# Kernel tuning notes

Hardware: AMD Instinct MI355X
Metric: run time of the kernel (lower is better)

Reference implementation:

```python
import jax, jax.numpy as jnp
import numpy as np

B, S, D, H, KV, HD = 2, 2048, 1024, 16, 4, 64
NUM_BUCKETS, MAX_DIST = 32, 128


def _rel_pos_bucket(rel_pos, num_buckets=NUM_BUCKETS, max_distance=MAX_DIST):
    # bidirectional (is_decoder=False) T5 bucketing
    nb = num_buckets // 2
    buckets = (rel_pos > 0).astype(jnp.int32) * nb
    rel = jnp.abs(rel_pos)
    max_exact = nb // 2
    is_small = rel < max_exact
    rel_f = jnp.maximum(rel, 1).astype(jnp.float32)
    large = max_exact + (
        jnp.log(rel_f / max_exact) / np.log(max_distance / max_exact) * (nb - max_exact)
    ).astype(jnp.int32)
    large = jnp.minimum(large, nb - 1)
    return buckets + jnp.where(is_small, rel, large)


def _pool_weight(W, scale, apply_scale):
    # W: [inner_dim, d_model] (torch Linear layout). Optionally scale per head,
    # group-sum heads into kv_heads, broadcast back to n_heads.
    Wh = W.reshape(H, HD, D)                       # [H, hd, D]
    if apply_scale:
        # torch path: W.T -> [D,H,hd] * scale[H,1] -> back; equivalent per-head scale
        Wh = Wh * scale[:, :, None]                # scale: [H,1] -> [H,1,1]
    Wg = Wh.reshape(KV, H // KV, HD, D).sum(axis=1)  # [KV, hd, D]
    Wb = jnp.repeat(Wg, H // KV, axis=0)           # [H, hd, D]
    return Wb.reshape(H * HD, D)


def setup_inputs() -> dict:
    key = jax.random.key(0)
    ks = jax.random.split(key, 8)
    s = 1.0 / np.sqrt(D)
    return {
        "hidden_states": jax.random.normal(ks[0], (B, S, D), jnp.float32),
        "Wq": jax.random.normal(ks[1], (H * HD, D), jnp.float32) * s,
        "Wk": jax.random.normal(ks[2], (H * HD, D), jnp.float32) * s,
        "Wv": jax.random.normal(ks[3], (H * HD, D), jnp.float32) * s,
        "Wo": jax.random.normal(ks[4], (D, H * HD), jnp.float32) * s,
        "key_scale": jax.random.normal(ks[5], (H, 1), jnp.float32),
        "value_scale": jax.random.normal(ks[6], (H, 1), jnp.float32),
        "bias_emb": jax.random.normal(ks[7], (NUM_BUCKETS, H), jnp.float32),
    }


def reference(hidden_states, Wq, Wk, Wv, Wo, key_scale, value_scale, bias_emb):
    x = hidden_states
    # Q projection -> [B, H, S, hd]
    q = (x @ Wq.T).reshape(B, S, H, HD).transpose(0, 2, 1, 3)

    # K weight: per-head scale applied, then pooled. V weight: the original code
    # computes the scaled version but then (bug, replicated faithfully) pools the
    # RAW v weight, so value_scale has no effect on the forward math.
    Wk_eff = _pool_weight(Wk, key_scale, apply_scale=True)
    Wv_eff = _pool_weight(Wv, value_scale, apply_scale=False)

    k = (x @ Wk_eff.T).reshape(B, S, H, HD).transpose(0, 2, 1, 3)
    v = (x @ Wv_eff.T).reshape(B, S, H, HD).transpose(0, 2, 1, 3)

    # T5 attention: no 1/sqrt(d) scaling
    scores = jnp.einsum("bhqd,bhkd->bhqk", q, k)  # [B,H,S,S]

    # relative position bias
    ctx = jnp.arange(S)[:, None]
    mem = jnp.arange(S)[None, :]
    buckets = _rel_pos_bucket(mem - ctx)            # [S, S]
    pos_bias = bias_emb[buckets]                    # [S, S, H]
    pos_bias = pos_bias.transpose(2, 0, 1)[None]    # [1, H, S, S]

    scores = scores + pos_bias
    attn = jax.nn.softmax(scores.astype(jnp.float32), axis=-1).astype(scores.dtype)
    out = jnp.einsum("bhqk,bhkd->bhqd", attn, v)    # [B,H,S,hd]
    out = out.transpose(0, 2, 1, 3).reshape(B, S, H * HD)
    return out @ Wo.T                               # [B, S, D]
```

## Files before the change

### kernel.cpp

```cpp
#include <hip/hip_runtime.h>

using half8  = __attribute__((ext_vector_type(8))) _Float16;
using half4  = __attribute__((ext_vector_type(4))) _Float16;
using half2v = __attribute__((ext_vector_type(2))) _Float16;
using fp16x2 = __attribute__((ext_vector_type(2))) __fp16;
using f32x4  = __attribute__((ext_vector_type(4))) float;

#define BB 2
#define SS 2048
#define DD 1024
#define HH 16
#define KVH 4
#define HDIM 64
#define NQK 1280
#define LOG2E 1.4426950408889634f

#define GLDS(g, l) __builtin_amdgcn_global_load_lds( \
    (const __attribute__((address_space(1))) void*)(g), \
    (__attribute__((address_space(3))) void*)(l), 16, 0, 0)

__device__ __forceinline__ f32x4 mfma16(half4 a, half4 b, f32x4 c) {
    return __builtin_amdgcn_mfma_f32_16x16x16f16(a, b, c, 0, 0, 0);
}

__device__ __forceinline__ float fexp2(float x) {
#if __has_builtin(__builtin_amdgcn_exp2f)
    return __builtin_amdgcn_exp2f(x);
#else
    return exp2f(x);
#endif
}

__device__ __forceinline__ half2v cvt_pk_f16(float a, float b) {
    fp16x2 r = __builtin_amdgcn_cvt_pkrtz(a, b);
    return __builtin_bit_cast(half2v, r);
}

__device__ __forceinline__ int kv_off(int row, int hcol) {
    return row * 64 + ((((hcol >> 3) ^ row) & 7) << 3) + (hcol & 7);
}

__device__ __forceinline__ int gm_off(int row, int slot) {
    return row * 32 + (((slot ^ row) & 3) << 3);
}

__device__ __forceinline__ int rel_large(int rel) {
    int n;
    if (rel < 12) n = 0; else if (rel < 16) n = 1; else if (rel < 23) n = 2;
    else if (rel < 32) n = 3; else if (rel < 46) n = 4; else if (rel < 64) n = 5;
    else if (rel < 91) n = 6; else if (rel < 128) n = 7; else n = 8;
    int large = 8 + n;
    return large > 15 ? 15 : large;
}

__global__ void prep_all(const float* __restrict__ x,
                         const float* __restrict__ Wq, const float* __restrict__ Wk,
                         const float* __restrict__ Wv, const float* __restrict__ Wo,
                         const float* __restrict__ ksc, const float* __restrict__ bias_emb,
                         _Float16* __restrict__ Wqk, _Float16* __restrict__ Wvb,
                         _Float16* __restrict__ Wob, float* __restrict__ tab,
                         _Float16* __restrict__ Xh)
{
    int bid = blockIdx.x;
    if (bid < 2560) {
        int row = bid;
        int c = threadIdx.x * 4;
        if (row < NQK) {
            if (row < 1024) {
                #pragma unroll
                for (int j = 0; j < 4; ++j)
                    Wqk[(size_t)row * DD + c + j] = (_Float16)(Wq[(size_t)row * DD + c + j] * LOG2E);
            } else {
                int kh = row - 1024;
                int kvi = kh >> 6, hd = kh & 63;
                #pragma unroll
                for (int j = 0; j < 4; ++j) {
                    float s = 0.f;
                    #pragma unroll
                    for (int g = 0; g < 4; ++g)
                        s += Wk[(size_t)((kvi * 4 + g) * 64 + hd) * DD + c + j] * ksc[kvi * 4 + g];
                    Wqk[(size_t)row * DD + c + j] = (_Float16)s;
                }
            }
        } else if (row < 1536) {
            int vh = row - 1280;
            int kvi = vh >> 6, hd = vh & 63;
            #pragma unroll
            for (int j = 0; j < 4; ++j) {
                float s = 0.f;
                #pragma unroll
                for (int g = 0; g < 4; ++g)
                    s += Wv[(size_t)((kvi * 4 + g) * 64 + hd) * DD + c + j];
                Wvb[(size_t)vh * DD + c + j] = (_Float16)s;
            }
        } else {
            int r = row - 1536;
            #pragma unroll
            for (int j = 0; j < 4; ++j)
                Wob[(size_t)r * DD + c + j] = (_Float16)Wo[(size_t)r * DD + c + j];
        }
    } else if (bid < 6656) {
        int idx = ((bid - 2560) * 256 + threadIdx.x) * 4;
        float4 v = *(const float4*)(x + idx);
        half4 o = { (_Float16)v.x, (_Float16)v.y, (_Float16)v.z, (_Float16)v.w };
        *(half4*)(Xh + idx) = o;
    } else {
        int idx = (bid - 6656) * 256 + threadIdx.x;
        if (idx < HH * 4095) {
            int h = idx / 4095;
            int dpos = idx % 4095;
            int d = dpos - 2047;
            int rel = d < 0 ? -d : d;
            int bucket = (rel < 8) ? rel : rel_large(rel);
            if (d > 0) bucket += 16;
            tab[(size_t)h * 4095 + dpos] = bias_emb[bucket * HH + h] * LOG2E;
        }
    }
}

template<int OUTK>
__global__ __launch_bounds__(256) void gemm_bt(const _Float16* __restrict__ A,
                                               const _Float16* __restrict__ B,
                                               void* __restrict__ C0,
                                               _Float16* __restrict__ C1,
                                               int M, int K, int ldc)
{
    __shared__ __align__(16) _Float16 As[2][64 * 32];
    __shared__ __align__(16) _Float16 Bs[2][128 * 32];

    int nwg = gridDim.x * gridDim.y;
    int lid = blockIdx.y * gridDim.x + blockIdx.x;
    int sid = (lid & 7) * (nwg >> 3) + (lid >> 3);
    int m0 = (sid / gridDim.x) * 64, n0 = (sid % gridDim.x) * 128;

    int t = threadIdx.x;
    int wv = t >> 6, lane = t & 63;
    int wm = wv >> 1, wn = wv & 1;
    int lr = lane & 15, lg = lane >> 4;
    int srow = lane >> 2;
    int scol = (((lane & 3) ^ (srow & 3)) << 3);
    f32x4 acc[2][4] = {};

#define GSTAGE(BUF, K0)                                                       \
    {                                                                         \
                         \
        GLDS(A + (size_t)(m0 + wv * 16 + srow) * K + (K0) + scol,             \
             &As[BUF][wv * 512 + lane * 8]);                                  \
        _Pragma("unroll")                                                     \
        for (int i_ = 0; i_ < 2; ++i_) {                                      \
            int chunk_ = wv * 2 + i_;                                         \
            GLDS(B + (size_t)(n0 + chunk_ * 16 + srow) * K + (K0) + scol,     \
                 &Bs[BUF][chunk_ * 512 + lane * 8]);                          \
        }                                                                     \
    }

    GSTAGE(0, 0);
    __syncthreads();
    int cur = 0;

    for (int k0 = 0; k0 < K; k0 += 32) {
        if (k0 + 32 < K) GSTAGE(cur ^ 1, k0 + 32);
        half8 af[2], bfr[4];
        #pragma unroll
        for (int mi = 0; mi < 2; ++mi)
            af[mi] = *(const half8*)(&As[cur][gm_off(wm * 32 + mi * 16 + lr, lg)]);
        #pragma unroll
        for (int ni = 0; ni < 4; ++ni)
            bfr[ni] = *(const half8*)(&Bs[cur][gm_off(wn * 64 + ni * 16 + lr, lg)]);
        __builtin_amdgcn_s_setprio(1);
        #pragma unroll
        for (int mi = 0; mi < 2; ++mi)
            #pragma unroll
            for (int ni = 0; ni < 4; ++ni)
                acc[mi][ni] = __builtin_amdgcn_mfma_f32_16x16x32_f16(af[mi], bfr[ni], acc[mi][ni], 0, 0, 0);
        __builtin_amdgcn_s_setprio(0);
        __syncthreads();
        cur ^= 1;
    }
#undef GSTAGE

    #pragma unroll
    for (int mi = 0; mi < 2; ++mi) {
        #pragma unroll
        for (int ni = 0; ni < 4; ++ni) {
            int rowb = m0 + wm * 32 + mi * 16 + 4 * lg;
            int col  = n0 + wn * 64 + ni * 16 + lr;
            if constexpr (OUTK == 0) {
                #pragma unroll
                for (int r = 0; r < 4; ++r)
                    ((float*)C0)[(size_t)(rowb + r) * ldc + col] = acc[mi][ni][r];
            } else {
                if (n0 < 1280) {
                    #pragma unroll
                    for (int r = 0; r < 4; ++r)
                        ((_Float16*)C0)[(size_t)(rowb + r) * ldc + col] = (_Float16)acc[mi][ni][r];
                } else {
                    half4 o = { (_Float16)acc[mi][ni][0], (_Float16)acc[mi][ni][1],
                                (_Float16)acc[mi][ni][2], (_Float16)acc[mi][ni][3] };
                    *(half4*)(C1 + (size_t)(col - 1280) * M + rowb) = o;
                }
            }
        }
    }
}

__global__ __launch_bounds__(512) void attn(const _Float16* __restrict__ Y,
                                            const _Float16* __restrict__ Vt,
                                            const float* __restrict__ tab,
                                            _Float16* __restrict__ O)
{
    int blk = (blockIdx.x & 7) * 64 + (blockIdx.x >> 3);
    int qb = blk & 15, h = (blk >> 4) & 15, b = blk >> 8;
    int kv = h >> 2;
    int q0 = qb * 128;
    int t = threadIdx.x, w = t >> 6, lane = t & 63, lr = lane & 15, lg = lane >> 4;

    __shared__ __align__(16) _Float16 Ks[2][64 * 64];
    __shared__ __align__(16) _Float16 Vst[2][64 * 64];
    __shared__ float bias_s[2][192];

    const size_t yoff = (size_t)(b * SS + q0 + w * 16 + lr) * NQK + h * 64;
    half8 aq0 = *(const half8*)(Y + yoff + lg * 8);
    half8 aq1 = *(const half8*)(Y + yoff + 32 + lg * 8);

    const float bias_neg = tab[(size_t)h * 4095 + 0];
    const float bias_pos = tab[(size_t)h * 4095 + 4094];

    f32x4 acc_o[4] = {};
    float m = -1e30f, l = 0.f;
    const int bb = 127 - w * 16 - lr + 4 * lg;

    uint4 kreg, vreg;
    float breg = 0.f;
    const int srow = t >> 3, sc8 = (t & 7) << 3;

#define FAR(K0) (((K0) >= q0 + 256) || ((K0) <= q0 - 192))

#define ATTN_LOAD(KEY0)                                                          \
    {                                                                            \
        int k0_ = (KEY0);                                                        \
        kreg = *(const uint4*)(Y + (size_t)(b * SS + k0_ + srow) * NQK + 1024 + kv * 64 + sc8); \
        vreg = *(const uint4*)(Vt + (size_t)(kv * 64 + srow) * 4096 + b * SS + k0_ + sc8); \
        if (!FAR(k0_) && t < 192) {                                              \
            int ti = k0_ - q0 + t + 1920;                                        \
            ti = ti < 0 ? 0 : (ti > 4094 ? 4094 : ti);                           \
            breg = tab[(size_t)h * 4095 + ti];                                   \
        }                                                                        \
    }

#define ATTN_WRITE(BUF, KEY0)                                                    \
    {                                                                            \
        int bf_ = (BUF);                                                         \
        *(uint4*)(&Ks[bf_][kv_off(srow, sc8)]) = kreg;                           \
        *(uint4*)(&Vst[bf_][kv_off(srow, sc8)]) = vreg;                          \
        if (!FAR(KEY0) && t < 192) bias_s[bf_][t] = breg;                        \
    }

    ATTN_LOAD(0);
    ATTN_WRITE(0, 0);
    __syncthreads();
    int cur = 0;

    for (int key0 = 0; key0 < SS; key0 += 64) {
        if (key0 + 64 < SS) ATTN_LOAD(key0 + 64);

        const _Float16* ks = Ks[cur];
        const _Float16* vs = Vst[cur];
        bool far = FAR(key0);

        f32x4 z = {0.f, 0.f, 0.f, 0.f};
        f32x4 sc[4];
        __builtin_amdgcn_s_setprio(1);
        #pragma unroll
        for (int dt = 0; dt < 4; ++dt) {
            half8 bk0 = *(const half8*)(&ks[kv_off(dt * 16 + lr, lg * 8)]);
            half8 bk1 = *(const half8*)(&ks[kv_off(dt * 16 + lr, 32 + lg * 8)]);
            sc[dt] = __builtin_amdgcn_mfma_f32_16x16x32_f16(bk0, aq0, z, 0, 0, 0);
            sc[dt] = __builtin_amdgcn_mfma_f32_16x16x32_f16(bk1, aq1, sc[dt], 0, 0, 0);
        }
        __builtin_amdgcn_s_setprio(0);

        float c;
        if (!far) {
            #pragma unroll
            for (int dt = 0; dt < 4; ++dt)
                #pragma unroll
                for (int r = 0; r < 4; ++r)
                    sc[dt][r] += bias_s[cur][bb + dt * 16 + r];
            c = 0.f;
        } else {
            c = (key0 > q0) ? bias_pos : bias_neg;
        }

        float pmax = sc[0][0];
        #pragma unroll
        for (int dt = 0; dt < 4; ++dt)
            #pragma unroll
            for (int r = 0; r < 4; ++r) pmax = fmaxf(pmax, sc[dt][r]);
        pmax = fmaxf(pmax, __shfl_xor(pmax, 16, 64));
        pmax = fmaxf(pmax, __shfl_xor(pmax, 32, 64));
        pmax += c;
        if (__any(pmax > m + 8.f)) {
            float mn = fmaxf(m, pmax);
            float scale = fexp2(m - mn);
            l *= scale;
            #pragma unroll
            for (int odt = 0; odt < 4; ++odt)
                #pragma unroll
                for (int r = 0; r < 4; ++r) acc_o[odt][r] *= scale;
            m = mn;
        }
        float moff = m - c;
        float rs = 0.f;
        #pragma unroll
        for (int dt = 0; dt < 4; ++dt)
            #pragma unroll
            for (int r = 0; r < 4; ++r) {
                float p = fexp2(sc[dt][r] - moff);
                sc[dt][r] = p;
                rs += p;
            }
        rs += __shfl_xor(rs, 16, 64);
        rs += __shfl_xor(rs, 32, 64);
        l += rs;

        half4 pf[4];
        #pragma unroll
        for (int dt = 0; dt < 4; ++dt) {
            half2v p01 = cvt_pk_f16(sc[dt][0], sc[dt][1]);
            half2v p23 = cvt_pk_f16(sc[dt][2], sc[dt][3]);
            pf[dt] = { p01[0], p01[1], p23[0], p23[1] };
        }

        __builtin_amdgcn_s_setprio(1);
        #pragma unroll
        for (int odt = 0; odt < 4; ++odt)
            #pragma unroll
            for (int dt = 0; dt < 4; ++dt) {
                half4 vf = *(const half4*)(&vs[kv_off(odt * 16 + lr, dt * 16 + 4 * lg)]);
                acc_o[odt] = mfma16(vf, pf[dt], acc_o[odt]);
            }
        __builtin_amdgcn_s_setprio(0);

        if (key0 + 64 < SS) {
            ATTN_WRITE(cur ^ 1, key0 + 64);
            __syncthreads();
            cur ^= 1;
        }
    }

    float inv = 1.f / l;
    _Float16* orow = O + (size_t)(b * SS + q0 + w * 16 + lr) * 1024 + h * 64;
    #pragma unroll
    for (int odt = 0; odt < 4; ++odt) {
        half4 o = { (_Float16)(acc_o[odt][0] * inv), (_Float16)(acc_o[odt][1] * inv),
                    (_Float16)(acc_o[odt][2] * inv), (_Float16)(acc_o[odt][3] * inv) };
        *(half4*)(orow + odt * 16 + 4 * lg) = o;
    }
#undef ATTN_LOAD
#undef ATTN_WRITE
#undef FAR
}

extern "C" void kernel_launch(void* const* d_in, const int* in_sizes, int n_in,
                              void* d_out, int out_size, void* d_ws, size_t ws_size,
                              hipStream_t stream)
{
    const float* x   = (const float*)d_in[0];
    const float* Wq  = (const float*)d_in[1];
    const float* Wk  = (const float*)d_in[2];
    const float* Wv  = (const float*)d_in[3];
    const float* Wo  = (const float*)d_in[4];
    const float* ksc = (const float*)d_in[5];
    const float* bias_emb = (const float*)d_in[7];
    float* out = (float*)d_out;

    char* ws = (char*)d_ws;
    _Float16* Wqk = (_Float16*)(ws);
    _Float16* Wvb = (_Float16*)(ws + 2621440);
    _Float16* Wob = (_Float16*)(ws + 3145728);
    float*    tab = (float*)(ws + 5242880);
    _Float16* Xh  = (_Float16*)(ws + 5505024);
    _Float16* Y   = (_Float16*)(ws + 13893632);
    _Float16* Vt  = (_Float16*)(ws + 24379392);
    _Float16* Ob  = (_Float16*)(ws + 26476544);

    prep_all<<<6912, 256, 0, stream>>>(x, Wq, Wk, Wv, Wo, ksc, bias_emb,
                                       Wqk, Wvb, Wob, tab, Xh);

    gemm_bt<3><<<dim3(12, 64), 256, 0, stream>>>(Xh, Wqk, Y, Vt, 4096, 1024, NQK);

    attn<<<512, 512, 0, stream>>>(Y, Vt, tab, Ob);

    gemm_bt<0><<<dim3(8, 64), 256, 0, stream>>>(Ob, Wob, out, nullptr, 4096, 1024, 1024);
}
```

Baseline: 116.9 us.

## Process two query tiles per warp in attention to reuse K/V LDS reads

The attention kernel now uses 256 threads (4 warps) per block, and each warp handles two 16-row query tiles, 64 rows apart, instead of one. Every K and V fragment read from LDS feeds two MFMAs, which halves LDS read traffic per unit of compute. Each thread now loads twice as much K/V data per tile into shared memory. The costs are higher register pressure from doubled accumulators and softmax state, and fewer warps available to hide latency.

```diff
diff --git a/kernel.cpp b/kernel.cpp
--- a/kernel.cpp
+++ b/kernel.cpp
@@ -204,7 +204,7 @@
     }
 }
 
-__global__ __launch_bounds__(512) void attn(const _Float16* __restrict__ Y,
+__global__ __launch_bounds__(256) void attn(const _Float16* __restrict__ Y,
                                             const _Float16* __restrict__ Vt,
                                             const float* __restrict__ tab,
                                             _Float16* __restrict__ O)
@@ -219,28 +219,36 @@
     __shared__ __align__(16) _Float16 Vst[2][64 * 64];
     __shared__ float bias_s[2][192];
 
-    const size_t yoff = (size_t)(b * SS + q0 + w * 16 + lr) * NQK + h * 64;
-    half8 aq0 = *(const half8*)(Y + yoff + lg * 8);
-    half8 aq1 = *(const half8*)(Y + yoff + 32 + lg * 8);
+    const size_t yoffA = (size_t)(b * SS + q0 + w * 16 + lr) * NQK + h * 64;
+    const size_t yoffB = yoffA + (size_t)64 * NQK;
+    half8 aq0a = *(const half8*)(Y + yoffA + lg * 8);
+    half8 aq1a = *(const half8*)(Y + yoffA + 32 + lg * 8);
+    half8 aq0b = *(const half8*)(Y + yoffB + lg * 8);
+    half8 aq1b = *(const half8*)(Y + yoffB + 32 + lg * 8);
 
     const float bias_neg = tab[(size_t)h * 4095 + 0];
     const float bias_pos = tab[(size_t)h * 4095 + 4094];
 
-    f32x4 acc_o[4] = {};
-    float m = -1e30f, l = 0.f;
-    const int bb = 127 - w * 16 - lr + 4 * lg;
-
-    uint4 kreg, vreg;
+    f32x4 acc_a[4] = {}, acc_b[4] = {};
+    float ma = -1e30f, la = 0.f, mb = -1e30f, lb = 0.f;
+    const int bbA = 127 - w * 16 - lr + 4 * lg;
+    const int bbB = bbA - 64;
+
+    uint4 kreg0, kreg1, vreg0, vreg1;
     float breg = 0.f;
-    const int srow = t >> 3, sc8 = (t & 7) << 3;
+    const int srow = t >> 2, scb = (t & 3) << 4;
 
 #define FAR(K0) (((K0) >= q0 + 256) || ((K0) <= q0 - 192))
 
 #define ATTN_LOAD(KEY0)                                                          \
     {                                                                            \
         int k0_ = (KEY0);                                                        \
-        kreg = *(const uint4*)(Y + (size_t)(b * SS + k0_ + srow) * NQK + 1024 + kv * 64 + sc8); \
-        vreg = *(const uint4*)(Vt + (size_t)(kv * 64 + srow) * 4096 + b * SS + k0_ + sc8); \
+        const _Float16* kp_ = Y + (size_t)(b * SS + k0_ + srow) * NQK + 1024 + kv * 64 + scb; \
+        kreg0 = *(const uint4*)(kp_);                                            \
+        kreg1 = *(const uint4*)(kp_ + 8);                                        \
+        const _Float16* vp_ = Vt + (size_t)(kv * 64 + srow) * 4096 + b * SS + k0_ + scb; \
+        vreg0 = *(const uint4*)(vp_);                                            \
+        vreg1 = *(const uint4*)(vp_ + 8);                                        \
         if (!FAR(k0_) && t < 192) {                                              \
             int ti = k0_ - q0 + t + 1920;                                        \
             ti = ti < 0 ? 0 : (ti > 4094 ? 4094 : ti);                           \
@@ -251,8 +259,10 @@
 #define ATTN_WRITE(BUF, KEY0)                                                    \
     {                                                                            \
         int bf_ = (BUF);                                                         \
-        *(uint4*)(&Ks[bf_][kv_off(srow, sc8)]) = kreg;                           \
-        *(uint4*)(&Vst[bf_][kv_off(srow, sc8)]) = vreg;                          \
+        *(uint4*)(&Ks[bf_][kv_off(srow, scb)]) = kreg0;                          \
+        *(uint4*)(&Ks[bf_][kv_off(srow, scb + 8)]) = kreg1;                      \
+        *(uint4*)(&Vst[bf_][kv_off(srow, scb)]) = vreg0;                         \
+        *(uint4*)(&Vst[bf_][kv_off(srow, scb + 8)]) = vreg1;                     \
         if (!FAR(KEY0) && t < 192) bias_s[bf_][t] = breg;                        \
     }
 
@@ -269,67 +279,109 @@
         bool far = FAR(key0);
 
         f32x4 z = {0.f, 0.f, 0.f, 0.f};
-        f32x4 sc[4];
+        f32x4 sa[4], sb[4];
         __builtin_amdgcn_s_setprio(1);
         #pragma unroll
         for (int dt = 0; dt < 4; ++dt) {
             half8 bk0 = *(const half8*)(&ks[kv_off(dt * 16 + lr, lg * 8)]);
             half8 bk1 = *(const half8*)(&ks[kv_off(dt * 16 + lr, 32 + lg * 8)]);
-            sc[dt] = __builtin_amdgcn_mfma_f32_16x16x32_f16(bk0, aq0, z, 0, 0, 0);
-            sc[dt] = __builtin_amdgcn_mfma_f32_16x16x32_f16(bk1, aq1, sc[dt], 0, 0, 0);
+            sa[dt] = __builtin_amdgcn_mfma_f32_16x16x32_f16(bk0, aq0a, z, 0, 0, 0);
+            sa[dt] = __builtin_amdgcn_mfma_f32_16x16x32_f16(bk1, aq1a, sa[dt], 0, 0, 0);
+            sb[dt] = __builtin_amdgcn_mfma_f32_16x16x32_f16(bk0, aq0b, z, 0, 0, 0);
+            sb[dt] = __builtin_amdgcn_mfma_f32_16x16x32_f16(bk1, aq1b, sb[dt], 0, 0, 0);
         }
         __builtin_amdgcn_s_setprio(0);
 
-        float c;
+        float ca, cb;
         if (!far) {
             #pragma unroll
             for (int dt = 0; dt < 4; ++dt)
                 #pragma unroll
-                for (int r = 0; r < 4; ++r)
-                    sc[dt][r] += bias_s[cur][bb + dt * 16 + r];
-            c = 0.f;
+                for (int r = 0; r < 4; ++r) {
+                    sa[dt][r] += bias_s[cur][bbA + dt * 16 + r];
+                    sb[dt][r] += bias_s[cur][bbB + dt * 16 + r];
+                }
+            ca = cb = 0.f;
         } else {
-            c = (key0 > q0) ? bias_pos : bias_neg;
-        }
-
-        float pmax = sc[0][0];
-        #pragma unroll
-        for (int dt = 0; dt < 4; ++dt)
-            #pragma unroll
-            for (int r = 0; r < 4; ++r) pmax = fmaxf(pmax, sc[dt][r]);
-        pmax = fmaxf(pmax, __shfl_xor(pmax, 16, 64));
-        pmax = fmaxf(pmax, __shfl_xor(pmax, 32, 64));
-        pmax += c;
-        if (__any(pmax > m + 8.f)) {
-            float mn = fmaxf(m, pmax);
-            float scale = fexp2(m - mn);
-            l *= scale;
-            #pragma unroll
-            for (int odt = 0; odt < 4; ++odt)
-                #pragma unroll
-                for (int r = 0; r < 4; ++r) acc_o[odt][r] *= scale;
-            m = mn;
-        }
-        float moff = m - c;
-        float rs = 0.f;
-        #pragma unroll
-        for (int dt = 0; dt < 4; ++dt)
-            #pragma unroll
-            for (int r = 0; r < 4; ++r) {
-                float p = fexp2(sc[dt][r] - moff);
-                sc[dt][r] = p;
-                rs += p;
-            }
-        rs += __shfl_xor(rs, 16, 64);
-        rs += __shfl_xor(rs, 32, 64);
-        l += rs;
-
-        half4 pf[4];
+            ca = cb = (key0 > q0) ? bias_pos : bias_neg;
+        }
+
+        {
+            float pmax = sa[0][0];
+            #pragma unroll
+            for (int dt = 0; dt < 4; ++dt)
+                #pragma unroll
+                for (int r = 0; r < 4; ++r) pmax = fmaxf(pmax, sa[dt][r]);
+            pmax = fmaxf(pmax, __shfl_xor(pmax, 16, 64));
+            pmax = fmaxf(pmax, __shfl_xor(pmax, 32, 64));
+            pmax += ca;
+            if (__any(pmax > ma + 8.f)) {
+                float mn = fmaxf(ma, pmax);
+                float scale = fexp2(ma - mn);
+                la *= scale;
+                #pragma unroll
+                for (int odt = 0; odt < 4; ++odt)
+                    #pragma unroll
+                    for (int r = 0; r < 4; ++r) acc_a[odt][r] *= scale;
+                ma = mn;
+            }
+            float moff = ma - ca;
+            float rs = 0.f;
+            #pragma unroll
+            for (int dt = 0; dt < 4; ++dt)
+                #pragma unroll
+                for (int r = 0; r < 4; ++r) {
+                    float p = fexp2(sa[dt][r] - moff);
+                    sa[dt][r] = p;
+                    rs += p;
+                }
+            rs += __shfl_xor(rs, 16, 64);
+            rs += __shfl_xor(rs, 32, 64);
+            la += rs;
+        }
+        {
+            float pmax = sb[0][0];
+            #pragma unroll
+            for (int dt = 0; dt < 4; ++dt)
+                #pragma unroll
+                for (int r = 0; r < 4; ++r) pmax = fmaxf(pmax, sb[dt][r]);
+            pmax = fmaxf(pmax, __shfl_xor(pmax, 16, 64));
+            pmax = fmaxf(pmax, __shfl_xor(pmax, 32, 64));
+            pmax += cb;
+            if (__any(pmax > mb + 8.f)) {
+                float mn = fmaxf(mb, pmax);
+                float scale = fexp2(mb - mn);
+                lb *= scale;
+                #pragma unroll
+                for (int odt = 0; odt < 4; ++odt)
+                    #pragma unroll
+                    for (int r = 0; r < 4; ++r) acc_b[odt][r] *= scale;
+                mb = mn;
+            }
+            float moff = mb - cb;
+            float rs = 0.f;
+            #pragma unroll
+            for (int dt = 0; dt < 4; ++dt)
+                #pragma unroll
+                for (int r = 0; r < 4; ++r) {
+                    float p = fexp2(sb[dt][r] - moff);
+                    sb[dt][r] = p;
+                    rs += p;
+                }
+            rs += __shfl_xor(rs, 16, 64);
+            rs += __shfl_xor(rs, 32, 64);
+            lb += rs;
+        }
+
+        half4 pfa[4], pfb[4];
         #pragma unroll
         for (int dt = 0; dt < 4; ++dt) {
-            half2v p01 = cvt_pk_f16(sc[dt][0], sc[dt][1]);
-            half2v p23 = cvt_pk_f16(sc[dt][2], sc[dt][3]);
-            pf[dt] = { p01[0], p01[1], p23[0], p23[1] };
+            half2v a01 = cvt_pk_f16(sa[dt][0], sa[dt][1]);
+            half2v a23 = cvt_pk_f16(sa[dt][2], sa[dt][3]);
+            pfa[dt] = { a01[0], a01[1], a23[0], a23[1] };
+            half2v b01 = cvt_pk_f16(sb[dt][0], sb[dt][1]);
+            half2v b23 = cvt_pk_f16(sb[dt][2], sb[dt][3]);
+            pfb[dt] = { b01[0], b01[1], b23[0], b23[1] };
         }
 
         __builtin_amdgcn_s_setprio(1);
@@ -338,7 +390,8 @@
             #pragma unroll
             for (int dt = 0; dt < 4; ++dt) {
                 half4 vf = *(const half4*)(&vs[kv_off(odt * 16 + lr, dt * 16 + 4 * lg)]);
-                acc_o[odt] = mfma16(vf, pf[dt], acc_o[odt]);
+                acc_a[odt] = mfma16(vf, pfa[dt], acc_a[odt]);
+                acc_b[odt] = mfma16(vf, pfb[dt], acc_b[odt]);
             }
         __builtin_amdgcn_s_setprio(0);
 
@@ -349,13 +402,17 @@
         }
     }
 
-    float inv = 1.f / l;
-    _Float16* orow = O + (size_t)(b * SS + q0 + w * 16 + lr) * 1024 + h * 64;
+    float inva = 1.f / la, invb = 1.f / lb;
+    _Float16* orowA = O + (size_t)(b * SS + q0 + w * 16 + lr) * 1024 + h * 64;
+    _Float16* orowB = orowA + (size_t)64 * 1024;
     #pragma unroll
     for (int odt = 0; odt < 4; ++odt) {
-        half4 o = { (_Float16)(acc_o[odt][0] * inv), (_Float16)(acc_o[odt][1] * inv),
-                    (_Float16)(acc_o[odt][2] * inv), (_Float16)(acc_o[odt][3] * inv) };
-        *(half4*)(orow + odt * 16 + 4 * lg) = o;
+        half4 oa = { (_Float16)(acc_a[odt][0] * inva), (_Float16)(acc_a[odt][1] * inva),
+                     (_Float16)(acc_a[odt][2] * inva), (_Float16)(acc_a[odt][3] * inva) };
+        *(half4*)(orowA + odt * 16 + 4 * lg) = oa;
+        half4 ob = { (_Float16)(acc_b[odt][0] * invb), (_Float16)(acc_b[odt][1] * invb),
+                     (_Float16)(acc_b[odt][2] * invb), (_Float16)(acc_b[odt][3] * invb) };
+        *(half4*)(orowB + odt * 16 + 4 * lg) = ob;
     }
 #undef ATTN_LOAD
 #undef ATTN_WRITE
@@ -390,7 +447,7 @@
 
     gemm_bt<3><<<dim3(12, 64), 256, 0, stream>>>(Xh, Wqk, Y, Vt, 4096, 1024, NQK);
 
-    attn<<<512, 512, 0, stream>>>(Y, Vt, tab, Ob);
+    attn<<<512, 256, 0, stream>>>(Y, Vt, tab, Ob);
 
     gemm_bt<0><<<dim3(8, 64), 256, 0, stream>>>(Ob, Wob, out, nullptr, 4096, 1024, 1024);
 }
```

Result: slower. 123.3 us (median of 2 runs) (+5.5%).

## Process two key tiles per barrier with four-buffer LDS pipeline in attention

Applied to the files above, without the earlier changes.

The attention loop now handles two 64-key tiles per iteration, prefetching the next two tiles into registers and writing them into a 4-slot LDS ring. This halves the number of __syncthreads barriers and gives global loads more compute to hide behind. The cost is double the LDS footprint for K/V/bias and extra live registers for the second prefetch, which may reduce occupancy.

```diff
diff --git a/kernel.cpp b/kernel.cpp
--- a/kernel.cpp
+++ b/kernel.cpp
@@ -215,9 +215,9 @@
     int q0 = qb * 128;
     int t = threadIdx.x, w = t >> 6, lane = t & 63, lr = lane & 15, lg = lane >> 4;
 
-    __shared__ __align__(16) _Float16 Ks[2][64 * 64];
-    __shared__ __align__(16) _Float16 Vst[2][64 * 64];
-    __shared__ float bias_s[2][192];
+    __shared__ __align__(16) _Float16 Ks[4][64 * 64];
+    __shared__ __align__(16) _Float16 Vst[4][64 * 64];
+    __shared__ float bias_s[4][192];
 
     const size_t yoff = (size_t)(b * SS + q0 + w * 16 + lr) * NQK + h * 64;
     half8 aq0 = *(const half8*)(Y + yoff + lg * 8);
@@ -230,42 +230,29 @@
     float m = -1e30f, l = 0.f;
     const int bb = 127 - w * 16 - lr + 4 * lg;
 
-    uint4 kreg, vreg;
-    float breg = 0.f;
+    uint4 kregA, vregA, kregB, vregB;
+    float bregA = 0.f, bregB = 0.f;
     const int srow = t >> 3, sc8 = (t & 7) << 3;
 
 #define FAR(K0) (((K0) >= q0 + 256) || ((K0) <= q0 - 192))
 
-#define ATTN_LOAD(KEY0)                                                          \
-    {                                                                            \
-        int k0_ = (KEY0);                                                        \
-        kreg = *(const uint4*)(Y + (size_t)(b * SS + k0_ + srow) * NQK + 1024 + kv * 64 + sc8); \
-        vreg = *(const uint4*)(Vt + (size_t)(kv * 64 + srow) * 4096 + b * SS + k0_ + sc8); \
-        if (!FAR(k0_) && t < 192) {                                              \
-            int ti = k0_ - q0 + t + 1920;                                        \
-            ti = ti < 0 ? 0 : (ti > 4094 ? 4094 : ti);                           \
-            breg = tab[(size_t)h * 4095 + ti];                                   \
-        }                                                                        \
-    }
-
-#define ATTN_WRITE(BUF, KEY0)                                                    \
-    {                                                                            \
-        int bf_ = (BUF);                                                         \
-        *(uint4*)(&Ks[bf_][kv_off(srow, sc8)]) = kreg;                           \
-        *(uint4*)(&Vst[bf_][kv_off(srow, sc8)]) = vreg;                          \
-        if (!FAR(KEY0) && t < 192) bias_s[bf_][t] = breg;                        \
-    }
-
-    ATTN_LOAD(0);
-    ATTN_WRITE(0, 0);
-    __syncthreads();
-    int cur = 0;
-
-    for (int key0 = 0; key0 < SS; key0 += 64) {
-        if (key0 + 64 < SS) ATTN_LOAD(key0 + 64);
-
-        const _Float16* ks = Ks[cur];
-        const _Float16* vs = Vst[cur];
+    auto LOAD = [&](int k0_, uint4& kreg, uint4& vreg, float& breg) {
+        kreg = *(const uint4*)(Y + (size_t)(b * SS + k0_ + srow) * NQK + 1024 + kv * 64 + sc8);
+        vreg = *(const uint4*)(Vt + (size_t)(kv * 64 + srow) * 4096 + b * SS + k0_ + sc8);
+        if (!FAR(k0_) && t < 192) {
+            int ti = k0_ - q0 + t + 1920;
+            ti = ti < 0 ? 0 : (ti > 4094 ? 4094 : ti);
+            breg = tab[(size_t)h * 4095 + ti];
+        }
+    };
+    auto WRITE = [&](int buf, int k0_, const uint4& kreg, const uint4& vreg, float breg) {
+        *(uint4*)(&Ks[buf][kv_off(srow, sc8)]) = kreg;
+        *(uint4*)(&Vst[buf][kv_off(srow, sc8)]) = vreg;
+        if (!FAR(k0_) && t < 192) bias_s[buf][t] = breg;
+    };
+    auto COMPUTE = [&](int key0, int buf) {
+        const _Float16* ks = Ks[buf];
+        const _Float16* vs = Vst[buf];
         bool far = FAR(key0);
 
         f32x4 z = {0.f, 0.f, 0.f, 0.f};
@@ -286,7 +273,7 @@
             for (int dt = 0; dt < 4; ++dt)
                 #pragma unroll
                 for (int r = 0; r < 4; ++r)
-                    sc[dt][r] += bias_s[cur][bb + dt * 16 + r];
+                    sc[dt][r] += bias_s[buf][bb + dt * 16 + r];
             c = 0.f;
         } else {
             c = (key0 > q0) ? bias_pos : bias_neg;
@@ -341,11 +328,28 @@
                 acc_o[odt] = mfma16(vf, pf[dt], acc_o[odt]);
             }
         __builtin_amdgcn_s_setprio(0);
-
-        if (key0 + 64 < SS) {
-            ATTN_WRITE(cur ^ 1, key0 + 64);
+    };
+
+    LOAD(0, kregA, vregA, bregA);
+    LOAD(64, kregB, vregB, bregB);
+    WRITE(0, 0, kregA, vregA, bregA);
+    WRITE(1, 64, kregB, vregB, bregB);
+    __syncthreads();
+    int p = 0;
+
+    for (int key0 = 0; key0 < SS; key0 += 128) {
+        bool more = (key0 + 128) < SS;
+        if (more) {
+            LOAD(key0 + 128, kregA, vregA, bregA);
+            LOAD(key0 + 192, kregB, vregB, bregB);
+        }
+        COMPUTE(key0, p * 2);
+        if (more) WRITE((p ^ 1) * 2, key0 + 128, kregA, vregA, bregA);
+        COMPUTE(key0 + 64, p * 2 + 1);
+        if (more) {
+            WRITE((p ^ 1) * 2 + 1, key0 + 192, kregB, vregB, bregB);
             __syncthreads();
-            cur ^= 1;
+            p ^= 1;
         }
     }
 
@@ -357,8 +361,6 @@
                     (_Float16)(acc_o[odt][2] * inv), (_Float16)(acc_o[odt][3] * inv) };
         *(half4*)(orow + odt * 16 + 4 * lg) = o;
     }
-#undef ATTN_LOAD
-#undef ATTN_WRITE
 #undef FAR
 }
 
```

Result: no change. 116.4 us (median of 2 runs) (-0.4%).
